# Optimization experiments

Hardware: AMD Instinct MI355X
Metric: run time of the kernel (lower is better)

Reference implementation:

```python
import jax, jax.numpy as jnp
import numpy as np

H = 1024  # hidden_features
I = 64    # input_dims
O = 2     # output_dims
T = 4096  # timesteps


def setup_inputs() -> dict:
    key = jax.random.key(0)
    ks = jax.random.split(key, 12)
    s = 1.0 / np.sqrt(H)  # torch LSTMCell/Linear init scale
    return {
        "x_in":  jax.random.normal(ks[0], (T, I), dtype=jnp.float32),
        "W_ih1": jax.random.uniform(ks[1], (4 * H, I), jnp.float32, -s, s),
        "W_hh1": jax.random.uniform(ks[2], (4 * H, H), jnp.float32, -s, s),
        "b_ih1": jax.random.uniform(ks[3], (4 * H,), jnp.float32, -s, s),
        "b_hh1": jax.random.uniform(ks[4], (4 * H,), jnp.float32, -s, s),
        "W_ih2": jax.random.uniform(ks[5], (4 * H, H), jnp.float32, -s, s),
        "W_hh2": jax.random.uniform(ks[6], (4 * H, H), jnp.float32, -s, s),
        "b_ih2": jax.random.uniform(ks[7], (4 * H,), jnp.float32, -s, s),
        "b_hh2": jax.random.uniform(ks[8], (4 * H,), jnp.float32, -s, s),
        "W_out": jax.random.uniform(ks[9], (O, H), jnp.float32, -s, s),
        "b_out": jax.random.uniform(ks[10], (O,), jnp.float32, -s, s),
    }


def _lstm_cell(x, h, c, W_ih, W_hh, b_ih, b_hh):
    # PyTorch LSTMCell gate order: i, f, g, o
    gates = x @ W_ih.T + b_ih + h @ W_hh.T + b_hh  # [4H]
    i, f, g, o = jnp.split(gates, 4)
    i = jax.nn.sigmoid(i)
    f = jax.nn.sigmoid(f)
    g = jnp.tanh(g)
    o = jax.nn.sigmoid(o)
    c_new = f * c + i * g
    h_new = o * jnp.tanh(c_new)
    return h_new, c_new


def reference(x_in, W_ih1, W_hh1, b_ih1, b_hh1,
              W_ih2, W_hh2, b_ih2, b_hh2, W_out, b_out):
    def step(carry, x_t):
        h1, c1, h2, c2 = carry
        h1, c1 = _lstm_cell(x_t, h1, c1, W_ih1, W_hh1, b_ih1, b_hh1)
        h2, c2 = _lstm_cell(h1, h2, c2, W_ih2, W_hh2, b_ih2, b_hh2)
        out = h2 @ W_out.T + b_out  # [O]
        return (h1, c1, h2, c2), out

    z = jnp.zeros((H,), dtype=x_in.dtype)
    init = (z, z, z, z)
    _, outputs = jax.lax.scan(step, init, x_in)  # outputs: [T, O]
    return outputs
```

## Files before the change

### kernel.cpp

```cpp
#include <hip/hip_runtime.h>
#include <math.h>


#define HID 1024
#define DIN 64
#define TSTEPS 4096
#define NWG 256
#define TPB 512

typedef unsigned long long u64;
typedef unsigned int u32;
typedef _Float16 f16x2 __attribute__((ext_vector_type(2)));
typedef __fp16   g16x2 __attribute__((ext_vector_type(2)));

#define H2_OFF 2048
#define WS_NEED_U64 (2048ull + 4097ull * 1024ull)
#define WS_NEED_BYTES (WS_NEED_U64 * 8ull)
#define WS_ZERO_BYTES 32768

#define WLDS_U4 (8 * 512)
#define H1S_OFF (WLDS_U4 * 16)
#define H2S_OFF (H1S_OFF + 640 * 4)
#define DYN_LDS_BYTES (H2S_OFF + 640 * 4)

__device__ __forceinline__ float sigmoid_f(float v) {
    return 1.0f / (1.0f + __expf(-v));
}
__device__ __forceinline__ float tanh_f(float v) {
    return 2.0f / (1.0f + __expf(-2.0f * v)) - 1.0f;
}

__device__ __forceinline__ void st_pair(u64* p, float h, u32 tag) {
    u64 pk = ((u64)tag << 32) | (u64)__float_as_uint(h);
    __hip_atomic_store(p, pk, __ATOMIC_RELAXED, __HIP_MEMORY_SCOPE_AGENT);
}
__device__ __forceinline__ u64 ld_pair(const u64* p) {
    return __hip_atomic_load(p, __ATOMIC_RELAXED, __HIP_MEMORY_SCOPE_AGENT);
}
#define PTAG(v) ((u32)((v) >> 32))
#define PVAL(v) (__uint_as_float((u32)(v)))

union U32H2 { u32 u; f16x2 h; g16x2 g; };

__device__ __forceinline__ u32 pk2(float a, float b) {
    U32H2 t; t.g = __builtin_amdgcn_cvt_pkrtz(a, b); return t.u;
}

#if defined(__has_builtin)
#if __has_builtin(__builtin_amdgcn_fdot2)
#define HAS_FDOT2 1
#endif
#endif

__device__ __forceinline__ float dot2f(u32 a, u32 b, float c) {
    U32H2 x, y; x.u = a; y.u = b;
#ifdef HAS_FDOT2
    return __builtin_amdgcn_fdot2(x.h, y.h, c, false);
#else
    float r = fmaf((float)x.h.x, (float)y.h.x, c);
    return fmaf((float)x.h.y, (float)y.h.y, r);
#endif
}

#define PIN_W1() asm volatile("" : "+v"(w1p0), "+v"(w1p1), "+v"(w1p2), \
    "+v"(w1p3), "+v"(w1p4), "+v"(w1p5), "+v"(w1p6), "+v"(w1p7), \
    "+v"(w1p8), "+v"(w1p9), "+v"(w1pA), "+v"(w1pB), \
    "+v"(w1pC), "+v"(w1pD), "+v"(w1pE), "+v"(w1pF))

#define ASTEP(j, P0, P1, P2, P3) do {                               \
    uint4 hv = *(const uint4*)(h1s + hbase + 4*(j));                \
    uint4 w2 = wlds[(j)*512 + tid];                                 \
    a0 = dot2f(hv.x, P0, a0); a1 = dot2f(hv.y, P1, a1);             \
    a0 = dot2f(hv.z, P2, a0); a1 = dot2f(hv.w, P3, a1);             \
    e0 = dot2f(hv.x, w2.x, e0); e1 = dot2f(hv.y, w2.y, e1);         \
    e0 = dot2f(hv.z, w2.z, e0); e1 = dot2f(hv.w, w2.w, e1);         \
} while (0)

#define BSTEP(j) do {                                               \
    uint4 gv = *(const uint4*)(h2s + hbase + 4*(j));                \
    uint4 w3 = wlds[(4+(j))*512 + tid];                             \
    e0 = dot2f(gv.x, w3.x, e0); e1 = dot2f(gv.y, w3.y, e1);         \
    e0 = dot2f(gv.z, w3.z, e0); e1 = dot2f(gv.w, w3.w, e1);         \
} while (0)

__global__ void
__attribute__((amdgpu_flat_work_group_size(TPB, TPB), amdgpu_waves_per_eu(2, 2)))
lstm_persistent(
    const float* __restrict__ x,
    const float* __restrict__ Wih1, const float* __restrict__ Whh1,
    const float* __restrict__ bih1, const float* __restrict__ bhh1,
    const float* __restrict__ Wih2, const float* __restrict__ Whh2,
    const float* __restrict__ bih2, const float* __restrict__ bhh2,
    const float* __restrict__ Wout, const float* __restrict__ bout,
    float* __restrict__ out, u64* __restrict__ ws, int use_hist)
{
    const int wg   = blockIdx.x;
    const int tid  = threadIdx.x;
    const int wave = tid >> 6;
    const int lane = tid & 63;
    const int gate = tid >> 7;
    const int rsub = (tid >> 5) & 3;
    const int c    = tid & 31;
    const int row  = gate * HID + (wg << 2) + rsub;
    const int kbase = c << 5;

    u64* h1t = ws;
    u64* h2t = ws + H2_OFF;

    extern __shared__ __align__(16) char smem[];
    uint4* wlds = (uint4*)smem;
    u32*   h1s  = (u32*)(smem + H1S_OFF);
    u32*   h2s  = (u32*)(smem + H2S_OFF);

    {
        const float4* q2 = (const float4*)(Wih2 + (size_t)row * HID + kbase);
        const float4* q3 = (const float4*)(Whh2 + (size_t)row * HID + kbase);
        #pragma unroll
        for (int j = 0; j < 4; ++j) {
            float4 qa = q2[2*j], qb = q2[2*j+1];
            wlds[j * 512 + tid] = make_uint4(pk2(qa.x, qa.y), pk2(qa.z, qa.w),
                                             pk2(qb.x, qb.y), pk2(qb.z, qb.w));
        }
        #pragma unroll
        for (int j = 0; j < 4; ++j) {
            float4 qa = q3[2*j], qb = q3[2*j+1];
            wlds[(4+j) * 512 + tid] = make_uint4(pk2(qa.x, qa.y), pk2(qa.z, qa.w),
                                                 pk2(qb.x, qb.y), pk2(qb.z, qb.w));
        }
    }

    const float4* p1 = (const float4*)(Whh1 + (size_t)row * HID + kbase);
    float4 f0 = p1[0], f1 = p1[1], f2 = p1[2], f3 = p1[3];
    float4 f4 = p1[4], f5 = p1[5], f6 = p1[6], f7 = p1[7];
    u32 w1p0 = pk2(f0.x, f0.y), w1p1 = pk2(f0.z, f0.w);
    u32 w1p2 = pk2(f1.x, f1.y), w1p3 = pk2(f1.z, f1.w);
    u32 w1p4 = pk2(f2.x, f2.y), w1p5 = pk2(f2.z, f2.w);
    u32 w1p6 = pk2(f3.x, f3.y), w1p7 = pk2(f3.z, f3.w);
    u32 w1p8 = pk2(f4.x, f4.y), w1p9 = pk2(f4.z, f4.w);
    u32 w1pA = pk2(f5.x, f5.y), w1pB = pk2(f5.z, f5.w);
    u32 w1pC = pk2(f6.x, f6.y), w1pD = pk2(f6.z, f6.w);
    u32 w1pE = pk2(f7.x, f7.y), w1pF = pk2(f7.z, f7.w);
    PIN_W1();

    const float2 wx = *(const float2*)(Wih1 + (size_t)row * DIN + (c << 1));
    const float bsum1 = bih1[row] + bhh1[row];
    const float bsum2 = bih2[row] + bhh2[row];

    __shared__ float g1[4][4], g2[4][4];
    __shared__ float c1s[4], c2s[4];
    __shared__ float red0[8], red1[8];
    if (tid < 4) { c1s[tid] = 0.0f; c2s[tid] = 0.0f; }

    const int sdst = 20 * (tid >> 4) + (tid & 15);
    const int hbase = 20 * c;

    __syncthreads();

    for (int p = 0; p <= TSTEPS; ++p) {
        const u64* h1p = h1t + (size_t)(p & 1) * 1024 + (tid << 1);
        const int h2row_c = (p > 0) ? (use_hist ? (p - 1) : ((p - 1) & 1)) : 0;
        const u64* h2p = h2t + (size_t)h2row_c * 1024 + (tid << 1);
        const u32 want1 = (u32)p;
        const u32 want2 = (p >= 2) ? (u32)p : 0u;

        const int tx = (p < TSTEPS) ? p : 0;
        const float2 xv = *(const float2*)(x + (size_t)tx * DIN + (c << 1));

        u64 v1a, v1b;
        {
            int guard = 0;
            for (;;) {
                v1a = ld_pair(h1p); v1b = ld_pair(h1p + 1);
                if ((PTAG(v1a) == want1) & (PTAG(v1b) == want1)) break;
                if (++guard > (1 << 17)) break;
            }
        }
        u64 v2a = ld_pair(h2p), v2b = ld_pair(h2p + 1);

        PIN_W1();

        h1s[sdst] = pk2(PVAL(v1a), PVAL(v1b));
        __syncthreads();

        float a0 = 0.f, a1 = 0.f, e0 = 0.f, e1 = 0.f;
        ASTEP(0, w1p0, w1p1, w1p2, w1p3);
        ASTEP(1, w1p4, w1p5, w1p6, w1p7);
        ASTEP(2, w1p8, w1p9, w1pA, w1pB);
        ASTEP(3, w1pC, w1pD, w1pE, w1pF);
        a0 = fmaf(wx.x, xv.x, a0);
        a1 = fmaf(wx.y, xv.y, a1);

        float accA = a0 + a1;
        accA += __shfl_xor(accA, 1);
        accA += __shfl_xor(accA, 2);
        accA += __shfl_xor(accA, 4);
        accA += __shfl_xor(accA, 8);
        accA += __shfl_xor(accA, 16);
        if (c == 0) {
            float vA = accA + bsum1;
            g1[gate][rsub] = (gate == 2) ? tanh_f(vA) : sigmoid_f(vA);
        }

        {
            int guard = 0;
            while (!((PTAG(v2a) == want2) & (PTAG(v2b) == want2))) {
                v2a = ld_pair(h2p); v2b = ld_pair(h2p + 1);
                if (++guard > (1 << 17)) break;
            }
        }
        float sb0 = PVAL(v2a), sb1 = PVAL(v2b);
        h2s[sdst] = pk2(sb0, sb1);
        __syncthreads();

        if (p < TSTEPS && tid < 4) {
            float iv = g1[0][tid], fv = g1[1][tid];
            float gv = g1[2][tid], ov = g1[3][tid];
            float cn = fv * c1s[tid] + iv * gv;
            c1s[tid] = cn;
            st_pair(h1t + (size_t)((p + 1) & 1) * 1024 + (wg << 2) + tid,
                    ov * tanh_f(cn), (u32)(p + 1));
        }

        BSTEP(0); BSTEP(1); BSTEP(2); BSTEP(3);

        float accB = e0 + e1;
        accB += __shfl_xor(accB, 1);
        accB += __shfl_xor(accB, 2);
        accB += __shfl_xor(accB, 4);
        accB += __shfl_xor(accB, 8);
        accB += __shfl_xor(accB, 16);
        if (c == 0) {
            float vB = accB + bsum2;
            g2[gate][rsub] = (gate == 2) ? tanh_f(vB) : sigmoid_f(vB);
        }
        __syncthreads();

        if (p >= 1 && tid >= 4 && tid < 8) {
            int u = tid - 4;
            float iv = g2[0][u], fv = g2[1][u];
            float gv = g2[2][u], ov = g2[3][u];
            float cn = fv * c2s[u] + iv * gv;
            c2s[u] = cn;
            const int wr = use_hist ? p : (p & 1);
            st_pair(h2t + (size_t)wr * 1024 + (wg << 2) + u,
                    ov * tanh_f(cn), (u32)(p + 1));
        }

        if (!use_hist && wg == 0 && p >= 2) {
            const float2 wo0 = *(const float2*)(Wout + (tid << 1));
            const float2 wo1 = *(const float2*)(Wout + HID + (tid << 1));
            float q0 = wo0.x * sb0 + wo0.y * sb1;
            float q1 = wo1.x * sb0 + wo1.y * sb1;
            #pragma unroll
            for (int m = 1; m < 64; m <<= 1) {
                q0 += __shfl_xor(q0, m);
                q1 += __shfl_xor(q1, m);
            }
            if (lane == 0) { red0[wave] = q0; red1[wave] = q1; }
            __syncthreads();
            if (tid == 0) {
                float o0 = bout[0], o1 = bout[1];
                #pragma unroll
                for (int w = 0; w < 8; ++w) { o0 += red0[w]; o1 += red1[w]; }
                out[2*(p-2)+0] = o0;
                out[2*(p-2)+1] = o1;
            }
            __syncthreads();
        }
    }

    if (use_hist) {
        const float2 wo0 = *(const float2*)(Wout + (tid << 1));
        const float2 wo1 = *(const float2*)(Wout + HID + (tid << 1));
        const float bo0 = bout[0], bo1 = bout[1];
        for (int i = 0; i < 16; ++i) {
            const int t = (wg << 4) + i;
            const u64* hp = h2t + (size_t)(t + 1) * 1024 + (tid << 1);
            const u32 want = (u32)(t + 2);
            u64 va, vb; int guard = 0;
            for (;;) {
                va = ld_pair(hp); vb = ld_pair(hp + 1);
                if ((PTAG(va) == want) && (PTAG(vb) == want)) break;
                if (++guard > (1 << 15)) break;
            }
            float h0 = PVAL(va), h1v = PVAL(vb);
            float q0 = wo0.x * h0 + wo0.y * h1v;
            float q1 = wo1.x * h0 + wo1.y * h1v;
            #pragma unroll
            for (int m = 1; m < 64; m <<= 1) {
                q0 += __shfl_xor(q0, m);
                q1 += __shfl_xor(q1, m);
            }
            if (lane == 0) { red0[wave] = q0; red1[wave] = q1; }
            __syncthreads();
            if (tid == 0) {
                float o0 = bo0, o1 = bo1;
                #pragma unroll
                for (int w = 0; w < 8; ++w) { o0 += red0[w]; o1 += red1[w]; }
                out[2*t+0] = o0;
                out[2*t+1] = o1;
            }
            __syncthreads();
        }
    } else if (wg == 0) {
        const float2 wo0 = *(const float2*)(Wout + (tid << 1));
        const float2 wo1 = *(const float2*)(Wout + HID + (tid << 1));
        const u64* hp = h2t + (size_t)(TSTEPS & 1) * 1024 + (tid << 1);
        const u32 want = (u32)(TSTEPS + 1);
        u64 va, vb; int guard = 0;
        for (;;) {
            va = ld_pair(hp); vb = ld_pair(hp + 1);
            if ((PTAG(va) == want) && (PTAG(vb) == want)) break;
            if (++guard > (1 << 15)) break;
        }
        float h0 = PVAL(va), h1v = PVAL(vb);
        float q0 = wo0.x * h0 + wo0.y * h1v;
        float q1 = wo1.x * h0 + wo1.y * h1v;
        #pragma unroll
        for (int m = 1; m < 64; m <<= 1) {
            q0 += __shfl_xor(q0, m);
            q1 += __shfl_xor(q1, m);
        }
        if (lane == 0) { red0[wave] = q0; red1[wave] = q1; }
        __syncthreads();
        if (tid == 0) {
            float o0 = bout[0], o1 = bout[1];
            #pragma unroll
            for (int w = 0; w < 8; ++w) { o0 += red0[w]; o1 += red1[w]; }
            out[2*(TSTEPS-1)+0] = o0;
            out[2*(TSTEPS-1)+1] = o1;
        }
    }
}

extern "C" void kernel_launch(void* const* d_in, const int* in_sizes, int n_in,
                              void* d_out, int out_size, void* d_ws, size_t ws_size,
                              hipStream_t stream)
{
    const float* x    = (const float*)d_in[0];
    const float* Wih1 = (const float*)d_in[1];
    const float* Whh1 = (const float*)d_in[2];
    const float* bih1 = (const float*)d_in[3];
    const float* bhh1 = (const float*)d_in[4];
    const float* Wih2 = (const float*)d_in[5];
    const float* Whh2 = (const float*)d_in[6];
    const float* bih2 = (const float*)d_in[7];
    const float* bhh2 = (const float*)d_in[8];
    const float* Wout = (const float*)d_in[9];
    const float* bout = (const float*)d_in[10];
    float* out = (float*)d_out;
    u64*   ws  = (u64*)d_ws;

    const int use_hist = (ws_size >= WS_NEED_BYTES) ? 1 : 0;

    (void)hipFuncSetAttribute((const void*)lstm_persistent,
                              hipFuncAttributeMaxDynamicSharedMemorySize,
                              DYN_LDS_BYTES);

    (void)hipMemsetAsync(d_ws, 0, WS_ZERO_BYTES, stream);

    hipLaunchKernelGGL(lstm_persistent, dim3(NWG), dim3(TPB), DYN_LDS_BYTES,
                       stream,
                       x, Wih1, Whh1, bih1, bhh1,
                       Wih2, Whh2, bih2, bhh2,
                       Wout, bout, out, ws, use_hist);
}
```

Measured before the change: 7.560 ms.

## Reorder per-step schedule so h1 publish precedes layer-2 input dot products

Splits the fused layer-1/layer-2 input dot loop so layer-1 gates are reduced and the new h1 is stored to global memory before the layer-2 W_ih dot products run. The wait on h2 moves after that work, which takes the h2 spin off the critical path of publishing h1 and shortens the cross-workgroup dependency chain. It also software-pipelines the h1 spin loop by issuing the next load before checking the previous one. The cost is an extra __syncthreads per step and longer live ranges for the hv registers.

```diff
diff --git a/kernel.cpp b/kernel.cpp
--- a/kernel.cpp
+++ b/kernel.cpp
@@ -67,13 +67,10 @@
     "+v"(w1p8), "+v"(w1p9), "+v"(w1pA), "+v"(w1pB), \
     "+v"(w1pC), "+v"(w1pD), "+v"(w1pE), "+v"(w1pF))
 
-#define ASTEP(j, P0, P1, P2, P3) do {                               \
-    uint4 hv = *(const uint4*)(h1s + hbase + 4*(j));                \
+#define A2STEP(j, HV) do {                                          \
     uint4 w2 = wlds[(j)*512 + tid];                                 \
-    a0 = dot2f(hv.x, P0, a0); a1 = dot2f(hv.y, P1, a1);             \
-    a0 = dot2f(hv.z, P2, a0); a1 = dot2f(hv.w, P3, a1);             \
-    e0 = dot2f(hv.x, w2.x, e0); e1 = dot2f(hv.y, w2.y, e1);         \
-    e0 = dot2f(hv.z, w2.z, e0); e1 = dot2f(hv.w, w2.w, e1);         \
+    e0 = dot2f(HV.x, w2.x, e0); e1 = dot2f(HV.y, w2.y, e1);         \
+    e0 = dot2f(HV.z, w2.z, e0); e1 = dot2f(HV.w, w2.w, e1);         \
 } while (0)
 
 #define BSTEP(j) do {                                               \
@@ -168,11 +165,15 @@
 
         u64 v1a, v1b;
         {
+            u64 pa = ld_pair(h1p), pb = ld_pair(h1p + 1);
             int guard = 0;
             for (;;) {
-                v1a = ld_pair(h1p); v1b = ld_pair(h1p + 1);
-                if ((PTAG(v1a) == want1) & (PTAG(v1b) == want1)) break;
-                if (++guard > (1 << 17)) break;
+                u64 na = ld_pair(h1p), nb = ld_pair(h1p + 1);
+                if ((PTAG(pa) == want1) & (PTAG(pb) == want1)) {
+                    v1a = pa; v1b = pb; break;
+                }
+                pa = na; pb = nb;
+                if (++guard > (1 << 17)) { v1a = na; v1b = nb; break; }
             }
         }
         u64 v2a = ld_pair(h2p), v2b = ld_pair(h2p + 1);
@@ -182,11 +183,19 @@
         h1s[sdst] = pk2(PVAL(v1a), PVAL(v1b));
         __syncthreads();
 
-        float a0 = 0.f, a1 = 0.f, e0 = 0.f, e1 = 0.f;
-        ASTEP(0, w1p0, w1p1, w1p2, w1p3);
-        ASTEP(1, w1p4, w1p5, w1p6, w1p7);
-        ASTEP(2, w1p8, w1p9, w1pA, w1pB);
-        ASTEP(3, w1pC, w1pD, w1pE, w1pF);
+        uint4 hv0 = *(const uint4*)(h1s + hbase + 0);
+        uint4 hv1 = *(const uint4*)(h1s + hbase + 4);
+        uint4 hv2 = *(const uint4*)(h1s + hbase + 8);
+        uint4 hv3 = *(const uint4*)(h1s + hbase + 12);
+        float a0 = 0.f, a1 = 0.f;
+        a0 = dot2f(hv0.x, w1p0, a0); a1 = dot2f(hv0.y, w1p1, a1);
+        a0 = dot2f(hv0.z, w1p2, a0); a1 = dot2f(hv0.w, w1p3, a1);
+        a0 = dot2f(hv1.x, w1p4, a0); a1 = dot2f(hv1.y, w1p5, a1);
+        a0 = dot2f(hv1.z, w1p6, a0); a1 = dot2f(hv1.w, w1p7, a1);
+        a0 = dot2f(hv2.x, w1p8, a0); a1 = dot2f(hv2.y, w1p9, a1);
+        a0 = dot2f(hv2.z, w1pA, a0); a1 = dot2f(hv2.w, w1pB, a1);
+        a0 = dot2f(hv3.x, w1pC, a0); a1 = dot2f(hv3.y, w1pD, a1);
+        a0 = dot2f(hv3.z, w1pE, a0); a1 = dot2f(hv3.w, w1pF, a1);
         a0 = fmaf(wx.x, xv.x, a0);
         a1 = fmaf(wx.y, xv.y, a1);
 
@@ -200,16 +209,6 @@
             float vA = accA + bsum1;
             g1[gate][rsub] = (gate == 2) ? tanh_f(vA) : sigmoid_f(vA);
         }
-
-        {
-            int guard = 0;
-            while (!((PTAG(v2a) == want2) & (PTAG(v2b) == want2))) {
-                v2a = ld_pair(h2p); v2b = ld_pair(h2p + 1);
-                if (++guard > (1 << 17)) break;
-            }
-        }
-        float sb0 = PVAL(v2a), sb1 = PVAL(v2b);
-        h2s[sdst] = pk2(sb0, sb1);
         __syncthreads();
 
         if (p < TSTEPS && tid < 4) {
@@ -220,6 +219,23 @@
             st_pair(h1t + (size_t)((p + 1) & 1) * 1024 + (wg << 2) + tid,
                     ov * tanh_f(cn), (u32)(p + 1));
         }
+
+        float e0 = 0.f, e1 = 0.f;
+        A2STEP(0, hv0);
+        A2STEP(1, hv1);
+        A2STEP(2, hv2);
+        A2STEP(3, hv3);
+
+        {
+            int guard = 0;
+            while (!((PTAG(v2a) == want2) & (PTAG(v2b) == want2))) {
+                v2a = ld_pair(h2p); v2b = ld_pair(h2p + 1);
+                if (++guard > (1 << 17)) break;
+            }
+        }
+        float sb0 = PVAL(v2a), sb1 = PVAL(v2b);
+        h2s[sdst] = pk2(sb0, sb1);
+        __syncthreads();
 
         BSTEP(0); BSTEP(1); BSTEP(2); BSTEP(3);
 
```

New measurement: 9.858 ms. 1.3x slower.

## Split workgroup into layer-1 and layer-2 halves with LDS counter sync

Applied to the files above, without the earlier changes.

Splits each 512-thread workgroup into two 256-thread halves: one runs the layer-1 recurrence with W_hh1 kept in registers, the other runs layer 2 with its weights in LDS. The halves replace __syncthreads with workgroup-scope atomic counters in shared memory, and the h1/h2 LDS staging is double-buffered. Layer-1 h values are packed as fp16 pairs in the global exchange, so each tagged word carries two values. The aim is to let layer 1 of the next step run concurrently with layer 2 and take workgroup barriers off the critical path. In exchange it adds spin-wait overhead, hand-placed waitcnt ordering and more complex hazard reasoning, and halves the lanes working on each dot product.

```diff
diff --git a/kernel.cpp b/kernel.cpp
--- a/kernel.cpp
+++ b/kernel.cpp
@@ -18,10 +18,15 @@
 #define WS_NEED_BYTES (WS_NEED_U64 * 8ull)
 #define WS_ZERO_BYTES 32768
 
-#define WLDS_U4 (8 * 512)
+#define WLDS_U4 4096
 #define H1S_OFF (WLDS_U4 * 16)
-#define H2S_OFF (H1S_OFF + 640 * 4)
-#define DYN_LDS_BYTES (H2S_OFF + 640 * 4)
+#define H2S_OFF (H1S_OFF + 2 * 640 * 4)
+#define DYN_LDS_BYTES (H2S_OFF + 2 * 640 * 4)
+
+#define ADR20(e) (20 * ((e) >> 4) + ((e) & 15))
+
+#define POLL_GUARD (1 << 18)
+#define SPIN_GUARD (1 << 19)
 
 __device__ __forceinline__ float sigmoid_f(float v) {
     return 1.0f / (1.0f + __expf(-v));
@@ -30,6 +35,9 @@
     return 2.0f / (1.0f + __expf(-2.0f * v)) - 1.0f;
 }
 
+__device__ __forceinline__ void st_u64(u64* p, u64 v) {
+    __hip_atomic_store(p, v, __ATOMIC_RELAXED, __HIP_MEMORY_SCOPE_AGENT);
+}
 __device__ __forceinline__ void st_pair(u64* p, float h, u32 tag) {
     u64 pk = ((u64)tag << 32) | (u64)__float_as_uint(h);
     __hip_atomic_store(p, pk, __ATOMIC_RELAXED, __HIP_MEMORY_SCOPE_AGENT);
@@ -40,8 +48,18 @@
 #define PTAG(v) ((u32)((v) >> 32))
 #define PVAL(v) (__uint_as_float((u32)(v)))
 
+__device__ __forceinline__ void bump(int* c) {
+    __hip_atomic_fetch_add(c, 1, __ATOMIC_RELEASE, __HIP_MEMORY_SCOPE_WORKGROUP);
+}
+__device__ __forceinline__ void spin_ge(int* c, int target) {
+    int g = 0;
+    while (__hip_atomic_load(c, __ATOMIC_ACQUIRE,
+                             __HIP_MEMORY_SCOPE_WORKGROUP) < target) {
+        if (++g > SPIN_GUARD) break;
+    }
+}
+
 union U32H2 { u32 u; f16x2 h; g16x2 g; };
-
 __device__ __forceinline__ u32 pk2(float a, float b) {
     U32H2 t; t.g = __builtin_amdgcn_cvt_pkrtz(a, b); return t.u;
 }
@@ -51,7 +69,6 @@
 #define HAS_FDOT2 1
 #endif
 #endif
-
 __device__ __forceinline__ float dot2f(u32 a, u32 b, float c) {
     U32H2 x, y; x.u = a; y.u = b;
 #ifdef HAS_FDOT2
@@ -62,26 +79,19 @@
 #endif
 }
 
-#define PIN_W1() asm volatile("" : "+v"(w1p0), "+v"(w1p1), "+v"(w1p2), \
-    "+v"(w1p3), "+v"(w1p4), "+v"(w1p5), "+v"(w1p6), "+v"(w1p7), \
-    "+v"(w1p8), "+v"(w1p9), "+v"(w1pA), "+v"(w1pB), \
-    "+v"(w1pC), "+v"(w1pD), "+v"(w1pE), "+v"(w1pF))
-
-#define ASTEP(j, P0, P1, P2, P3) do {                               \
-    uint4 hv = *(const uint4*)(h1s + hbase + 4*(j));                \
-    uint4 w2 = wlds[(j)*512 + tid];                                 \
-    a0 = dot2f(hv.x, P0, a0); a1 = dot2f(hv.y, P1, a1);             \
-    a0 = dot2f(hv.z, P2, a0); a1 = dot2f(hv.w, P3, a1);             \
-    e0 = dot2f(hv.x, w2.x, e0); e1 = dot2f(hv.y, w2.y, e1);         \
-    e0 = dot2f(hv.z, w2.z, e0); e1 = dot2f(hv.w, w2.w, e1);         \
-} while (0)
-
-#define BSTEP(j) do {                                               \
-    uint4 gv = *(const uint4*)(h2s + hbase + 4*(j));                \
-    uint4 w3 = wlds[(4+(j))*512 + tid];                             \
-    e0 = dot2f(gv.x, w3.x, e0); e1 = dot2f(gv.y, w3.y, e1);         \
-    e0 = dot2f(gv.z, w3.z, e0); e1 = dot2f(gv.w, w3.w, e1);         \
-} while (0)
+__device__ __forceinline__ uint4 pack4(float4 a, float4 b) {
+    return make_uint4(pk2(a.x, a.y), pk2(a.z, a.w),
+                      pk2(b.x, b.y), pk2(b.z, b.w));
+}
+
+#define PIN8() asm volatile("" : "+v"(qw0.x), "+v"(qw0.y), "+v"(qw0.z), \
+    "+v"(qw0.w), "+v"(qw1.x), "+v"(qw1.y), "+v"(qw1.z), "+v"(qw1.w),    \
+    "+v"(qw2.x), "+v"(qw2.y), "+v"(qw2.z), "+v"(qw2.w),                 \
+    "+v"(qw3.x), "+v"(qw3.y), "+v"(qw3.z), "+v"(qw3.w));                \
+    asm volatile("" : "+v"(qw4.x), "+v"(qw4.y), "+v"(qw4.z),            \
+    "+v"(qw4.w), "+v"(qw5.x), "+v"(qw5.y), "+v"(qw5.z), "+v"(qw5.w),    \
+    "+v"(qw6.x), "+v"(qw6.y), "+v"(qw6.z), "+v"(qw6.w),                 \
+    "+v"(qw7.x), "+v"(qw7.y), "+v"(qw7.z), "+v"(qw7.w))
 
 __global__ void
 __attribute__((amdgpu_flat_work_group_size(TPB, TPB), amdgpu_waves_per_eu(2, 2)))
@@ -96,13 +106,13 @@
 {
     const int wg   = blockIdx.x;
     const int tid  = threadIdx.x;
-    const int wave = tid >> 6;
-    const int lane = tid & 63;
-    const int gate = tid >> 7;
-    const int rsub = (tid >> 5) & 3;
-    const int c    = tid & 31;
-    const int row  = gate * HID + (wg << 2) + rsub;
-    const int kbase = c << 5;
+    const int half = tid >> 8;
+    const int rt   = tid & 255;
+    const int rrow = rt >> 4;
+    const int cc   = rt & 15;
+    const int gate = rrow >> 2;
+    const int rs   = rrow & 3;
+    const int R    = gate * HID + (wg << 2) + rs;
 
     u64* h1t = ws;
     u64* h2t = ws + H2_OFF;
@@ -112,162 +122,249 @@
     u32*   h1s  = (u32*)(smem + H1S_OFF);
     u32*   h2s  = (u32*)(smem + H2S_OFF);
 
-    {
-        const float4* q2 = (const float4*)(Wih2 + (size_t)row * HID + kbase);
-        const float4* q3 = (const float4*)(Whh2 + (size_t)row * HID + kbase);
+    __shared__ float g1buf[2][16], g2buf[2][16];
+    __shared__ float red0[8], red1[8];
+    __shared__ float redF0[2][4], redF1[2][4];
+    __shared__ int cnt1, cnt1g, cons1, cons1R, cnt2, cnt2g, cons2, cntO;
+
+    if (tid == 0) {
+        cnt1 = 0; cnt1g = 0; cons1 = 0; cons1R = 0;
+        cnt2 = 0; cnt2g = 0; cons2 = 0; cntO = 0;
+    }
+
+    if (half == 1) {
+        const float4* q2 = (const float4*)(Wih2 + (size_t)R * HID + (cc << 6));
+        const float4* q3 = (const float4*)(Whh2 + (size_t)R * HID + (cc << 6));
         #pragma unroll
-        for (int j = 0; j < 4; ++j) {
-            float4 qa = q2[2*j], qb = q2[2*j+1];
-            wlds[j * 512 + tid] = make_uint4(pk2(qa.x, qa.y), pk2(qa.z, qa.w),
-                                             pk2(qb.x, qb.y), pk2(qb.z, qb.w));
-        }
+        for (int j = 0; j < 8; ++j)
+            wlds[(j << 8) + rt] = pack4(q2[2*j], q2[2*j+1]);
         #pragma unroll
-        for (int j = 0; j < 4; ++j) {
-            float4 qa = q3[2*j], qb = q3[2*j+1];
-            wlds[(4+j) * 512 + tid] = make_uint4(pk2(qa.x, qa.y), pk2(qa.z, qa.w),
-                                                 pk2(qb.x, qb.y), pk2(qb.z, qb.w));
-        }
+        for (int j = 0; j < 8; ++j)
+            wlds[2048 + (j << 8) + rt] = pack4(q3[2*j], q3[2*j+1]);
     }
-
-    const float4* p1 = (const float4*)(Whh1 + (size_t)row * HID + kbase);
-    float4 f0 = p1[0], f1 = p1[1], f2 = p1[2], f3 = p1[3];
-    float4 f4 = p1[4], f5 = p1[5], f6 = p1[6], f7 = p1[7];
-    u32 w1p0 = pk2(f0.x, f0.y), w1p1 = pk2(f0.z, f0.w);
-    u32 w1p2 = pk2(f1.x, f1.y), w1p3 = pk2(f1.z, f1.w);
-    u32 w1p4 = pk2(f2.x, f2.y), w1p5 = pk2(f2.z, f2.w);
-    u32 w1p6 = pk2(f3.x, f3.y), w1p7 = pk2(f3.z, f3.w);
-    u32 w1p8 = pk2(f4.x, f4.y), w1p9 = pk2(f4.z, f4.w);
-    u32 w1pA = pk2(f5.x, f5.y), w1pB = pk2(f5.z, f5.w);
-    u32 w1pC = pk2(f6.x, f6.y), w1pD = pk2(f6.z, f6.w);
-    u32 w1pE = pk2(f7.x, f7.y), w1pF = pk2(f7.z, f7.w);
-    PIN_W1();
-
-    const float2 wx = *(const float2*)(Wih1 + (size_t)row * DIN + (c << 1));
-    const float bsum1 = bih1[row] + bhh1[row];
-    const float bsum2 = bih2[row] + bhh2[row];
-
-    __shared__ float g1[4][4], g2[4][4];
-    __shared__ float c1s[4], c2s[4];
-    __shared__ float red0[8], red1[8];
-    if (tid < 4) { c1s[tid] = 0.0f; c2s[tid] = 0.0f; }
-
-    const int sdst = 20 * (tid >> 4) + (tid & 15);
-    const int hbase = 20 * c;
-
     __syncthreads();
 
-    for (int p = 0; p <= TSTEPS; ++p) {
-        const u64* h1p = h1t + (size_t)(p & 1) * 1024 + (tid << 1);
-        const int h2row_c = (p > 0) ? (use_hist ? (p - 1) : ((p - 1) & 1)) : 0;
-        const u64* h2p = h2t + (size_t)h2row_c * 1024 + (tid << 1);
-        const u32 want1 = (u32)p;
-        const u32 want2 = (p >= 2) ? (u32)p : 0u;
-
-        const int tx = (p < TSTEPS) ? p : 0;
-        const float2 xv = *(const float2*)(x + (size_t)tx * DIN + (c << 1));
-
-        u64 v1a, v1b;
-        {
-            int guard = 0;
-            for (;;) {
-                v1a = ld_pair(h1p); v1b = ld_pair(h1p + 1);
-                if ((PTAG(v1a) == want1) & (PTAG(v1b) == want1)) break;
-                if (++guard > (1 << 17)) break;
-            }
-        }
-        u64 v2a = ld_pair(h2p), v2b = ld_pair(h2p + 1);
-
-        PIN_W1();
-
-        h1s[sdst] = pk2(PVAL(v1a), PVAL(v1b));
-        __syncthreads();
-
-        float a0 = 0.f, a1 = 0.f, e0 = 0.f, e1 = 0.f;
-        ASTEP(0, w1p0, w1p1, w1p2, w1p3);
-        ASTEP(1, w1p4, w1p5, w1p6, w1p7);
-        ASTEP(2, w1p8, w1p9, w1pA, w1pB);
-        ASTEP(3, w1pC, w1pD, w1pE, w1pF);
-        a0 = fmaf(wx.x, xv.x, a0);
-        a1 = fmaf(wx.y, xv.y, a1);
-
-        float accA = a0 + a1;
-        accA += __shfl_xor(accA, 1);
-        accA += __shfl_xor(accA, 2);
-        accA += __shfl_xor(accA, 4);
-        accA += __shfl_xor(accA, 8);
-        accA += __shfl_xor(accA, 16);
-        if (c == 0) {
-            float vA = accA + bsum1;
-            g1[gate][rsub] = (gate == 2) ? tanh_f(vA) : sigmoid_f(vA);
-        }
-
-        {
-            int guard = 0;
-            while (!((PTAG(v2a) == want2) & (PTAG(v2b) == want2))) {
-                v2a = ld_pair(h2p); v2b = ld_pair(h2p + 1);
-                if (++guard > (1 << 17)) break;
-            }
-        }
-        float sb0 = PVAL(v2a), sb1 = PVAL(v2b);
-        h2s[sdst] = pk2(sb0, sb1);
-        __syncthreads();
-
-        if (p < TSTEPS && tid < 4) {
-            float iv = g1[0][tid], fv = g1[1][tid];
-            float gv = g1[2][tid], ov = g1[3][tid];
-            float cn = fv * c1s[tid] + iv * gv;
-            c1s[tid] = cn;
-            st_pair(h1t + (size_t)((p + 1) & 1) * 1024 + (wg << 2) + tid,
-                    ov * tanh_f(cn), (u32)(p + 1));
-        }
-
-        BSTEP(0); BSTEP(1); BSTEP(2); BSTEP(3);
-
-        float accB = e0 + e1;
-        accB += __shfl_xor(accB, 1);
-        accB += __shfl_xor(accB, 2);
-        accB += __shfl_xor(accB, 4);
-        accB += __shfl_xor(accB, 8);
-        accB += __shfl_xor(accB, 16);
-        if (c == 0) {
-            float vB = accB + bsum2;
-            g2[gate][rsub] = (gate == 2) ? tanh_f(vB) : sigmoid_f(vB);
-        }
-        __syncthreads();
-
-        if (p >= 1 && tid >= 4 && tid < 8) {
-            int u = tid - 4;
-            float iv = g2[0][u], fv = g2[1][u];
-            float gv = g2[2][u], ov = g2[3][u];
-            float cn = fv * c2s[u] + iv * gv;
-            c2s[u] = cn;
-            const int wr = use_hist ? p : (p & 1);
-            st_pair(h2t + (size_t)wr * 1024 + (wg << 2) + u,
-                    ov * tanh_f(cn), (u32)(p + 1));
-        }
-
-        if (!use_hist && wg == 0 && p >= 2) {
-            const float2 wo0 = *(const float2*)(Wout + (tid << 1));
-            const float2 wo1 = *(const float2*)(Wout + HID + (tid << 1));
-            float q0 = wo0.x * sb0 + wo0.y * sb1;
-            float q1 = wo1.x * sb0 + wo1.y * sb1;
+    if (half == 0) {
+        const float4* p1 = (const float4*)(Whh1 + (size_t)R * HID + (cc << 6));
+        uint4 qw0 = pack4(p1[0],  p1[1]);
+        uint4 qw1 = pack4(p1[2],  p1[3]);
+        uint4 qw2 = pack4(p1[4],  p1[5]);
+        uint4 qw3 = pack4(p1[6],  p1[7]);
+        uint4 qw4 = pack4(p1[8],  p1[9]);
+        uint4 qw5 = pack4(p1[10], p1[11]);
+        uint4 qw6 = pack4(p1[12], p1[13]);
+        uint4 qw7 = pack4(p1[14], p1[15]);
+        PIN8();
+        const float4 wx4 = *(const float4*)(Wih1 + (size_t)R * DIN + (cc << 2));
+        const float bs1 = bih1[R] + bhh1[R];
+        float cA = 0.f, cB = 0.f;
+
+        for (int s = 0; s <= TSTEPS; ++s) {
+            const int buf = s & 1;
+            u32* hb = h1s + buf * 640;
+
+            if (s >= 3) spin_ge(&cons1, 4*(s-2));
+            if (s >= 2) spin_ge(&cons1R, 4*(s-1));
+
+            u32 pay1 = 0, pay2 = 0;
+            if (s > 0) {
+                const u64* hp = h1t + (size_t)buf * 512;
+                const u32 want = (u32)s;
+                u64 va = ld_pair(hp + rt), vb = ld_pair(hp + rt + 256);
+                int guard = 0;
+                while ((PTAG(va) != want) | (PTAG(vb) != want)) {
+                    if (PTAG(va) != want) va = ld_pair(hp + rt);
+                    if (PTAG(vb) != want) vb = ld_pair(hp + rt + 256);
+                    if (++guard > POLL_GUARD) break;
+                }
+                pay1 = (u32)va; pay2 = (u32)vb;
+            }
+
+            hb[ADR20(rt)]       = pay1;
+            hb[ADR20(rt) + 320] = pay2;
+            asm volatile("s_waitcnt lgkmcnt(0)" ::: "memory");
+            if ((rt & 63) == 0) bump(&cnt1);
+
+            if (s == TSTEPS) break;
+
+            spin_ge(&cnt1, 4*(s+1));
+            const float4 xv4 = *(const float4*)(x + (size_t)s * DIN + (cc << 2));
+
+            float a0 = 0.f, a1 = 0.f;
+            {
+                const u32* hbb = hb + 40 * cc;
+                uint4 hv;
+                hv = *(const uint4*)(hbb + 0);
+                a0 = dot2f(hv.x, qw0.x, a0); a1 = dot2f(hv.y, qw0.y, a1);
+                a0 = dot2f(hv.z, qw0.z, a0); a1 = dot2f(hv.w, qw0.w, a1);
+                hv = *(const uint4*)(hbb + 4);
+                a0 = dot2f(hv.x, qw1.x, a0); a1 = dot2f(hv.y, qw1.y, a1);
+                a0 = dot2f(hv.z, qw1.z, a0); a1 = dot2f(hv.w, qw1.w, a1);
+                hv = *(const uint4*)(hbb + 8);
+                a0 = dot2f(hv.x, qw2.x, a0); a1 = dot2f(hv.y, qw2.y, a1);
+                a0 = dot2f(hv.z, qw2.z, a0); a1 = dot2f(hv.w, qw2.w, a1);
+                hv = *(const uint4*)(hbb + 12);
+                a0 = dot2f(hv.x, qw3.x, a0); a1 = dot2f(hv.y, qw3.y, a1);
+                a0 = dot2f(hv.z, qw3.z, a0); a1 = dot2f(hv.w, qw3.w, a1);
+                hv = *(const uint4*)(hbb + 20);
+                a0 = dot2f(hv.x, qw4.x, a0); a1 = dot2f(hv.y, qw4.y, a1);
+                a0 = dot2f(hv.z, qw4.z, a0); a1 = dot2f(hv.w, qw4.w, a1);
+                hv = *(const uint4*)(hbb + 24);
+                a0 = dot2f(hv.x, qw5.x, a0); a1 = dot2f(hv.y, qw5.y, a1);
+                a0 = dot2f(hv.z, qw5.z, a0); a1 = dot2f(hv.w, qw5.w, a1);
+                hv = *(const uint4*)(hbb + 28);
+                a0 = dot2f(hv.x, qw6.x, a0); a1 = dot2f(hv.y, qw6.y, a1);
+                a0 = dot2f(hv.z, qw6.z, a0); a1 = dot2f(hv.w, qw6.w, a1);
+                hv = *(const uint4*)(hbb + 32);
+                a0 = dot2f(hv.x, qw7.x, a0); a1 = dot2f(hv.y, qw7.y, a1);
+                a0 = dot2f(hv.z, qw7.z, a0); a1 = dot2f(hv.w, qw7.w, a1);
+            }
+            asm volatile("s_waitcnt lgkmcnt(0)" ::: "memory");
+            if ((rt & 63) == 0) bump(&cons1R);
+
+            a0 = fmaf(wx4.x, xv4.x, a0); a1 = fmaf(wx4.y, xv4.y, a1);
+            a0 = fmaf(wx4.z, xv4.z, a0); a1 = fmaf(wx4.w, xv4.w, a1);
+            float accA = a0 + a1;
+            accA += __shfl_xor(accA, 1);
+            accA += __shfl_xor(accA, 2);
+            accA += __shfl_xor(accA, 4);
+            accA += __shfl_xor(accA, 8);
+            if (cc == 0) {
+                float vA = accA + bs1;
+                g1buf[buf][rrow] = (gate == 2) ? tanh_f(vA) : sigmoid_f(vA);
+            }
+            asm volatile("s_waitcnt lgkmcnt(0)" ::: "memory");
+            if ((rt & 63) == 0) bump(&cnt1g);
+
+            if (rt < 2) {
+                spin_ge(&cnt1g, 4*(s+1));
+                const float* gb = g1buf[buf];
+                const int u0 = rt << 1;
+                float i0 = gb[u0],   fv0 = gb[4+u0], g0 = gb[8+u0],  o0 = gb[12+u0];
+                float i1 = gb[u0+1], fv1 = gb[5+u0], g1x = gb[9+u0], o1 = gb[13+u0];
+                cA = fv0 * cA + i0 * g0;
+                cB = fv1 * cB + i1 * g1x;
+                float h0  = o0 * tanh_f(cA);
+                float h1v = o1 * tanh_f(cB);
+                u64 pkv = ((u64)(u32)(s + 1) << 32) | (u64)pk2(h0, h1v);
+                st_u64(h1t + (size_t)((s + 1) & 1) * 512 + (wg << 1) + rt, pkv);
+            }
+            PIN8();
+        }
+    } else {
+        const float bs2 = bih2[R] + bhh2[R];
+        float c2r = 0.f;
+        const float2 wa0 = *(const float2*)(Wout + (rt << 1));
+        const float2 wa1 = *(const float2*)(Wout + 512 + (rt << 1));
+        const float2 wb0 = *(const float2*)(Wout + HID + (rt << 1));
+        const float2 wb1 = *(const float2*)(Wout + HID + 512 + (rt << 1));
+
+        for (int t = 0; t < TSTEPS; ++t) {
+            const int bufK = t & 1;
+            const int bufH = (t + 1) & 1;
+            u32* h1b = h1s + bufH * 640;
+            u32* h2b = h2s + bufK * 640;
+
+            if (t >= 2) spin_ge(&cons2, 4*(t-1));
+
+            float v0 = 0.f, v1 = 0.f, v2 = 0.f, v3 = 0.f;
+            if (t > 0) {
+                const u64* hp = h2t +
+                    (size_t)(use_hist ? (t - 1) : ((t - 1) & 1)) * 1024;
+                const u32 want = (u32)t;
+                u64 a = ld_pair(hp + 2*rt),        b = ld_pair(hp + 2*rt + 1);
+                u64 cq = ld_pair(hp + 2*rt + 512), d = ld_pair(hp + 2*rt + 513);
+                int guard = 0;
+                while ((PTAG(a) != want) | (PTAG(b) != want) |
+                       (PTAG(cq) != want) | (PTAG(d) != want)) {
+                    if (PTAG(a) != want)  a  = ld_pair(hp + 2*rt);
+                    if (PTAG(b) != want)  b  = ld_pair(hp + 2*rt + 1);
+                    if (PTAG(cq) != want) cq = ld_pair(hp + 2*rt + 512);
+                    if (PTAG(d) != want)  d  = ld_pair(hp + 2*rt + 513);
+                    if (++guard > POLL_GUARD) break;
+                }
+                v0 = PVAL(a); v1 = PVAL(b); v2 = PVAL(cq); v3 = PVAL(d);
+            }
+
+            h2b[ADR20(rt)]       = pk2(v0, v1);
+            h2b[ADR20(rt) + 320] = pk2(v2, v3);
+            asm volatile("s_waitcnt lgkmcnt(0)" ::: "memory");
+            if ((rt & 63) == 0) bump(&cnt2);
+
+            spin_ge(&cnt1, 4*(t+2));
+            spin_ge(&cnt2, 4*(t+1));
+
+            float e0 = 0.f, e1 = 0.f;
+            const u32* hA = h1b + 40 * cc;
+            const u32* hB = h2b + 40 * cc;
             #pragma unroll
-            for (int m = 1; m < 64; m <<= 1) {
-                q0 += __shfl_xor(q0, m);
-                q1 += __shfl_xor(q1, m);
-            }
-            if (lane == 0) { red0[wave] = q0; red1[wave] = q1; }
-            __syncthreads();
-            if (tid == 0) {
-                float o0 = bout[0], o1 = bout[1];
+            for (int j = 0; j < 8; ++j) {
+                const int off = 20 * (j >> 2) + 4 * (j & 3);
+                uint4 hv = *(const uint4*)(hA + off);
+                uint4 w2 = wlds[(j << 8) + rt];
+                e0 = dot2f(hv.x, w2.x, e0); e1 = dot2f(hv.y, w2.y, e1);
+                e0 = dot2f(hv.z, w2.z, e0); e1 = dot2f(hv.w, w2.w, e1);
+            }
+            #pragma unroll
+            for (int j = 0; j < 8; ++j) {
+                const int off = 20 * (j >> 2) + 4 * (j & 3);
+                uint4 gv = *(const uint4*)(hB + off);
+                uint4 w3 = wlds[2048 + (j << 8) + rt];
+                e0 = dot2f(gv.x, w3.x, e0); e1 = dot2f(gv.y, w3.y, e1);
+                e0 = dot2f(gv.z, w3.z, e0); e1 = dot2f(gv.w, w3.w, e1);
+            }
+            asm volatile("s_waitcnt lgkmcnt(0)" ::: "memory");
+            if ((rt & 63) == 0) { bump(&cons1); bump(&cons2); }
+
+            float accB = e0 + e1;
+            accB += __shfl_xor(accB, 1);
+            accB += __shfl_xor(accB, 2);
+            accB += __shfl_xor(accB, 4);
+            accB += __shfl_xor(accB, 8);
+            if (cc == 0) {
+                float vB = accB + bs2;
+                g2buf[bufK][rrow] = (gate == 2) ? tanh_f(vB) : sigmoid_f(vB);
+            }
+            asm volatile("s_waitcnt lgkmcnt(0)" ::: "memory");
+            if ((rt & 63) == 0) bump(&cnt2g);
+
+            if (rt < 4) {
+                spin_ge(&cnt2g, 4*(t+1));
+                const float* gb = g2buf[bufK];
+                float iv = gb[rt], fv = gb[4+rt], gv2 = gb[8+rt], ov = gb[12+rt];
+                c2r = fv * c2r + iv * gv2;
+                float hh = ov * tanh_f(c2r);
+                const int wr = use_hist ? t : (t & 1);
+                st_pair(h2t + (size_t)wr * 1024 + (wg << 2) + rt, hh, (u32)(t + 1));
+            }
+
+            if (!use_hist && wg == 0 && t >= 1) {
+                float q0 = wa0.x*v0 + wa0.y*v1 + wa1.x*v2 + wa1.y*v3;
+                float q1 = wb0.x*v0 + wb0.y*v1 + wb1.x*v2 + wb1.y*v3;
                 #pragma unroll
-                for (int w = 0; w < 8; ++w) { o0 += red0[w]; o1 += red1[w]; }
-                out[2*(p-2)+0] = o0;
-                out[2*(p-2)+1] = o1;
-            }
-            __syncthreads();
+                for (int m = 1; m < 64; m <<= 1) {
+                    q0 += __shfl_xor(q0, m);
+                    q1 += __shfl_xor(q1, m);
+                }
+                const int wv = rt >> 6;
+                if ((rt & 63) == 0) { redF0[bufK][wv] = q0; redF1[bufK][wv] = q1; }
+                asm volatile("s_waitcnt lgkmcnt(0)" ::: "memory");
+                if ((rt & 63) == 0) bump(&cntO);
+                if (rt == 0) {
+                    spin_ge(&cntO, 4*t);
+                    float o0 = bout[0], o1 = bout[1];
+                    #pragma unroll
+                    for (int w = 0; w < 4; ++w) {
+                        o0 += redF0[bufK][w]; o1 += redF1[bufK][w];
+                    }
+                    out[2*(t-1)+0] = o0;
+                    out[2*(t-1)+1] = o1;
+                }
+            }
         }
     }
+
+    __syncthreads();
 
     if (use_hist) {
         const float2 wo0 = *(const float2*)(Wout + (tid << 1));
@@ -275,8 +372,8 @@
         const float bo0 = bout[0], bo1 = bout[1];
         for (int i = 0; i < 16; ++i) {
             const int t = (wg << 4) + i;
-            const u64* hp = h2t + (size_t)(t + 1) * 1024 + (tid << 1);
-            const u32 want = (u32)(t + 2);
+            const u64* hp = h2t + (size_t)t * 1024 + (tid << 1);
+            const u32 want = (u32)(t + 1);
             u64 va, vb; int guard = 0;
             for (;;) {
                 va = ld_pair(hp); vb = ld_pair(hp + 1);
@@ -291,7 +388,7 @@
                 q0 += __shfl_xor(q0, m);
                 q1 += __shfl_xor(q1, m);
             }
-            if (lane == 0) { red0[wave] = q0; red1[wave] = q1; }
+            if ((tid & 63) == 0) { red0[tid >> 6] = q0; red1[tid >> 6] = q1; }
             __syncthreads();
             if (tid == 0) {
                 float o0 = bo0, o1 = bo1;
@@ -305,8 +402,8 @@
     } else if (wg == 0) {
         const float2 wo0 = *(const float2*)(Wout + (tid << 1));
         const float2 wo1 = *(const float2*)(Wout + HID + (tid << 1));
-        const u64* hp = h2t + (size_t)(TSTEPS & 1) * 1024 + (tid << 1);
-        const u32 want = (u32)(TSTEPS + 1);
+        const u64* hp = h2t + (size_t)((TSTEPS - 1) & 1) * 1024 + (tid << 1);
+        const u32 want = (u32)TSTEPS;
         u64 va, vb; int guard = 0;
         for (;;) {
             va = ld_pair(hp); vb = ld_pair(hp + 1);
@@ -321,7 +418,7 @@
             q0 += __shfl_xor(q0, m);
             q1 += __shfl_xor(q1, m);
         }
-        if (lane == 0) { red0[wave] = q0; red1[wave] = q1; }
+        if ((tid & 63) == 0) { red0[tid >> 6] = q0; red1[tid >> 6] = q1; }
         __syncthreads();
         if (tid == 0) {
             float o0 = bout[0], o1 = bout[1];
```

Measured after the change: 14.25 ms. 88.5% more time.
